# Optimization experiments

Measured on AMD Instinct MI355X. Metric: run time of the kernel, lower is better.

Reference implementation:

```python
import jax, jax.numpy as jnp
import numpy as np

NUM_EMBEDDINGS = 1024
EMBEDDING_DIM = 256


def setup_inputs() -> dict:
    key = jax.random.key(0)
    k1, k2 = jax.random.split(key)
    z = jax.random.normal(k1, (32, EMBEDDING_DIM, 32, 32), dtype=jnp.float32)
    codebook = jax.random.normal(k2, (NUM_EMBEDDINGS, EMBEDDING_DIM), dtype=jnp.float32)
    return {"z": z, "codebook": codebook}


def reference(z, codebook):
    # z: (B, C, H, W) -> (B, H, W, C) -> (B*H*W, C)
    B, C, H, W = z.shape
    z_bhwc = jnp.transpose(z, (0, 2, 3, 1))
    z_flat = z_bhwc.reshape(-1, C)  # (N, C)

    # pairwise squared distances: ||z||^2 + ||e||^2 - 2 z.e^T  -> (N, K)
    distances = (
        jnp.sum(z_flat ** 2, axis=1, keepdims=True)
        + jnp.sum(codebook ** 2, axis=1)
        - 2.0 * jnp.matmul(z_flat, codebook.T)
    )
    argmin_codewords = jnp.argmin(distances, axis=1)  # (N,)
    min_codewords = jax.nn.one_hot(argmin_codewords, NUM_EMBEDDINGS, dtype=jnp.float32)  # (N, K)

    # quantized latents via one-hot @ codebook, back to (B, C, H, W)
    z_quantized = jnp.matmul(min_codewords, codebook).reshape(B, H, W, C)
    z_quantized = jnp.transpose(z_quantized, (0, 3, 1, 2))
    return (min_codewords, z_quantized)
```

## Files before the change

kernel.cpp:

```cpp
#include <hip/hip_runtime.h>

#define N_ROWS 32768
#define K_CODES 1024
#define CDIM 256

typedef _Float16 half8 __attribute__((ext_vector_type(8)));
typedef _Float16 half4 __attribute__((ext_vector_type(4)));
typedef float floatx16 __attribute__((ext_vector_type(16)));
typedef unsigned long long ull;

#define WS_ZH   0ull
#define WS_ZL   16777216ull
#define WS_CBH  33554432ull
#define WS_CBL  34078720ull
#define WS_CBN  34603008ull
#define WS_PART 34607104ull
#define WS_IDX  36704256ull
#define WS_NEED 36835328ull

__device__ __forceinline__ void g2lds16(const void* g, void* l) {
    __builtin_amdgcn_global_load_lds(
        (const __attribute__((address_space(1))) void*)g,
        (__attribute__((address_space(3))) void*)l, 16, 0, 0);
}

__global__ __launch_bounds__(256) void prep_all(const float* __restrict__ z,
                                                const float* __restrict__ cb,
                                                _Float16* __restrict__ zh,
                                                _Float16* __restrict__ zl,
                                                _Float16* __restrict__ cbh,
                                                _Float16* __restrict__ cbl,
                                                float* __restrict__ cbn) {
    __shared__ float t[64][68];
    if (blockIdx.x >= 2048) {
        int k = ((blockIdx.x - 2048) << 2) | (threadIdx.x >> 6);
        int lane = threadIdx.x & 63;
        float4 v = reinterpret_cast<const float4*>(cb + k * CDIM)[lane];
        float s0 = v.x * 32.f, s1 = v.y * 32.f, s2 = v.z * 32.f, s3 = v.w * 32.f;
        half4 hv, lv;
        hv[0] = (_Float16)s0; lv[0] = (_Float16)(s0 - (float)hv[0]);
        hv[1] = (_Float16)s1; lv[1] = (_Float16)(s1 - (float)hv[1]);
        hv[2] = (_Float16)s2; lv[2] = (_Float16)(s2 - (float)hv[2]);
        hv[3] = (_Float16)s3; lv[3] = (_Float16)(s3 - (float)hv[3]);
        size_t off = (size_t)((lane >> 1) * K_CODES + k) * 8 + ((lane & 1) * 4);
        *reinterpret_cast<half4*>(&cbh[off]) = hv;
        *reinterpret_cast<half4*>(&cbl[off]) = lv;
        float s = s0 * s0 + s1 * s1 + s2 * s2 + s3 * s3;
        #pragma unroll
        for (int off2 = 32; off2 > 0; off2 >>= 1) s += __shfl_down(s, off2);
        if (lane == 0) cbn[k] = s;
        return;
    }
    int hwt = blockIdx.x & 15;
    int ct  = (blockIdx.x >> 4) & 3;
    int bb  = blockIdx.x >> 6;
    int tid = threadIdx.x;
    #pragma unroll
    for (int p = 0; p < 4; p++) {
        int e = p * 256 + tid;
        int c = e >> 4, h4 = e & 15;
        float4 v = *reinterpret_cast<const float4*>(
            &z[((bb * 256 + ct * 64 + c) << 10) + hwt * 64 + h4 * 4]);
        *reinterpret_cast<float4*>(&t[c][h4 * 4]) = v;
    }
    __syncthreads();
    #pragma unroll
    for (int p = 0; p < 4; p++) {
        int e = p * 256 + tid;
        int hw = e >> 4, c4 = e & 15;
        half4 hv, lv;
        #pragma unroll
        for (int j = 0; j < 4; j++) {
            float s = t[c4 * 4 + j][hw] * 32.f;
            _Float16 h = (_Float16)s;
            hv[j] = h;
            lv[j] = (_Float16)(s - (float)h);
        }
        int n = bb * 1024 + hwt * 64 + hw;
        int cg = ct * 64 + c4 * 4;
        size_t off = (size_t)((cg >> 3) * N_ROWS + n) * 8 + (cg & 7);
        *reinterpret_cast<half4*>(&zh[off]) = hv;
        *reinterpret_cast<half4*>(&zl[off]) = lv;
    }
}

__global__ __launch_bounds__(256, 4) void vq_mfma32(
    const _Float16* __restrict__ zh, const _Float16* __restrict__ zl,
    const _Float16* __restrict__ cbh, const _Float16* __restrict__ cbl,
    const float* __restrict__ cbn, ull* __restrict__ partial) {

    __shared__ _Float16 AhL[4096], AlL[4096], BhL[4096], BlL[4096];
    __shared__ float rvv[128][2];
    __shared__ int   rcc[128][2];

    const int tid = threadIdx.x;
    const int lane = tid & 63, wave = tid >> 6;
    const int wm = wave & 1, wn = wave >> 1;
    const int fm = lane & 31, fq = lane >> 5;
    const int L = (blockIdx.x & 7) * 256 + (blockIdx.x >> 3);
    const int codeTile = L & 7;
    const int rowTile  = L >> 3;
    const int rowBase = rowTile * 128, codeBase = codeTile * 128;

    floatx16 acc[4];
    #pragma unroll
    for (int i = 0; i < 4; i++) acc[i] = (floatx16)0.f;

    for (int cc = 0; cc < 8; cc++) {
        #pragma unroll
        for (int i = 0; i < 2; i++) {
            int G = i * 256 + tid;
            int q = G >> 7, r = G & 127;
            size_t ao = ((size_t)(cc * 4 + q) * N_ROWS + rowBase + r) * 8;
            size_t bo = ((size_t)(cc * 4 + q) * K_CODES + codeBase + r) * 8;
            g2lds16(zh + ao,  &AhL[G * 8]);
            g2lds16(zl + ao,  &AlL[G * 8]);
            g2lds16(cbh + bo, &BhL[G * 8]);
            g2lds16(cbl + bo, &BlL[G * 8]);
        }
        __syncthreads();
        #pragma unroll
        for (int s = 0; s < 2; s++) {
            int q = s * 2 + fq;
            half8 ah[2], al[2], bh[2], bl[2];
            #pragma unroll
            for (int i = 0; i < 2; i++) {
                int ga = q * 128 + wm * 64 + i * 32 + fm;
                ah[i] = *reinterpret_cast<const half8*>(&AhL[ga * 8]);
                al[i] = *reinterpret_cast<const half8*>(&AlL[ga * 8]);
            }
            #pragma unroll
            for (int j = 0; j < 2; j++) {
                int gb = q * 128 + wn * 64 + j * 32 + fm;
                bh[j] = *reinterpret_cast<const half8*>(&BhL[gb * 8]);
                bl[j] = *reinterpret_cast<const half8*>(&BlL[gb * 8]);
            }
            #pragma unroll
            for (int i = 0; i < 2; i++)
                #pragma unroll
                for (int j = 0; j < 2; j++) {
                    acc[i*2+j] = __builtin_amdgcn_mfma_f32_32x32x16_f16(ah[i], bh[j], acc[i*2+j], 0, 0, 0);
                    acc[i*2+j] = __builtin_amdgcn_mfma_f32_32x32x16_f16(al[i], bh[j], acc[i*2+j], 0, 0, 0);
                    acc[i*2+j] = __builtin_amdgcn_mfma_f32_32x32x16_f16(ah[i], bl[j], acc[i*2+j], 0, 0, 0);
                }
        }
        __syncthreads();
    }

    float cbnv[2];
    #pragma unroll
    for (int j = 0; j < 2; j++) cbnv[j] = cbn[codeBase + wn * 64 + j * 32 + fm];

    #pragma unroll
    for (int i = 0; i < 2; i++)
        #pragma unroll
        for (int r = 0; r < 16; r++) {
            float best = 3.4e38f; int bcode = 0x7fffffff;
            #pragma unroll
            for (int j = 0; j < 2; j++) {
                float d = fmaf(-2.f, acc[i*2+j][r], cbnv[j]);
                int code = codeBase + wn * 64 + j * 32 + fm;
                if (d < best) { best = d; bcode = code; }
            }
            #pragma unroll
            for (int m = 1; m < 32; m <<= 1) {
                float ov = __shfl_xor(best, m, 64);
                int   oc = __shfl_xor(bcode, m, 64);
                if (ov < best || (ov == best && oc < bcode)) { best = ov; bcode = oc; }
            }
            if (fm == 0) {
                int row = wm * 64 + i * 32 + (r & 3) + 8 * (r >> 2) + 4 * fq;
                rvv[row][wn] = best;
                rcc[row][wn] = bcode;
            }
        }
    __syncthreads();
    if (tid < 128) {
        float v0 = rvv[tid][0]; int c0 = rcc[tid][0];
        float v1 = rvv[tid][1]; int c1 = rcc[tid][1];
        if (v1 < v0 || (v1 == v0 && c1 < c0)) { v0 = v1; c0 = c1; }
        unsigned u = __float_as_uint(v0);
        u = (u & 0x80000000u) ? ~u : (u | 0x80000000u);
        partial[(size_t)(rowBase + tid) * 8 + codeTile] =
            ((ull)u << 32) | (unsigned)c0;
    }
}

__global__ __launch_bounds__(256) void onehot_fin2(const ull* __restrict__ partial,
                                                   int* __restrict__ idx,
                                                   float* __restrict__ out) {
    __shared__ int sid[16];
    const int rb = blockIdx.x * 16;
    const int tid = threadIdx.x;
    if (tid < 128) {
        ull v = partial[(size_t)rb * 8 + tid];
        #pragma unroll
        for (int m = 1; m < 8; m <<= 1) {
            ull o = __shfl_xor(v, m, 64);
            if (o < v) v = o;
        }
        if ((tid & 7) == 0) {
            int r = tid >> 3;
            int id = (int)(v & 0xffffffffu);
            sid[r] = id;
            idx[rb + r] = id;
        }
    }
    __syncthreads();
    const int k4 = tid << 2;
    #pragma unroll
    for (int r = 0; r < 16; r++) {
        int id = sid[r];
        float4 v4;
        v4.x = (k4     == id) ? 1.f : 0.f;
        v4.y = (k4 + 1 == id) ? 1.f : 0.f;
        v4.z = (k4 + 2 == id) ? 1.f : 0.f;
        v4.w = (k4 + 3 == id) ? 1.f : 0.f;
        reinterpret_cast<float4*>(out)[(size_t)(rb + r) * 256 + tid] = v4;
    }
}

__global__ __launch_bounds__(256) void zq_fill2(const int* __restrict__ idx,
                                                const float* __restrict__ cb,
                                                float* __restrict__ out) {
    __shared__ float tile[64][257];
    const int tid = threadIdx.x;
    const int n0 = (blockIdx.x >> 2) << 8;
    const int c0 = (blockIdx.x & 3) << 6;
    const int b  = n0 >> 10;
    const int hw0 = n0 & 1023;

    const int id = idx[n0 + tid];
    const float4* cb4 = reinterpret_cast<const float4*>(cb);
    #pragma unroll
    for (int jj = 0; jj < 16; jj++) {
        float4 v = cb4[id * 64 + (c0 >> 2) + jj];
        tile[jj * 4 + 0][tid] = v.x;
        tile[jj * 4 + 1][tid] = v.y;
        tile[jj * 4 + 2][tid] = v.z;
        tile[jj * 4 + 3][tid] = v.w;
    }
    __syncthreads();
    #pragma unroll
    for (int c = 0; c < 64; c++) {
        out[((size_t)(b * 256 + c0 + c) << 10) + hw0 + tid] = tile[c][tid];
    }
}


__global__ __launch_bounds__(64) void cb_norms(const float* __restrict__ cb,
                                               float* __restrict__ cbn) {
    int k = blockIdx.x;
    int lane = threadIdx.x;
    float4 v = reinterpret_cast<const float4*>(cb + k * CDIM)[lane];
    float s = v.x * v.x + v.y * v.y + v.z * v.z + v.w * v.w;
    #pragma unroll
    for (int off = 32; off > 0; off >>= 1) s += __shfl_down(s, off);
    if (lane == 0) cbn[k] = s;
}

__global__ __launch_bounds__(256) void cb_transpose(const float* __restrict__ cb,
                                                    float* __restrict__ cbt) {
    __shared__ float t[32][33];
    int k0 = (blockIdx.x & 31) * 32;
    int c0 = (blockIdx.x >> 5) * 32;
    int lane = threadIdx.x & 31;
    int row = threadIdx.x >> 5;
    #pragma unroll
    for (int s = 0; s < 4; s++) {
        int r = row + s * 8;
        t[r][lane] = cb[(k0 + r) * CDIM + c0 + lane];
    }
    __syncthreads();
    #pragma unroll
    for (int s = 0; s < 4; s++) {
        int r = row + s * 8;
        cbt[(c0 + r) * K_CODES + k0 + lane] = t[lane][r];
    }
}

__global__ __launch_bounds__(512, 2) void vq_argmin(const float* __restrict__ z,
                                                    const float* __restrict__ cbt,
                                                    const float* __restrict__ cbn,
                                                    int* __restrict__ idx_out) {
    __shared__ float As[64][128];
    __shared__ float Bs[64][256];

    const int tid = threadIdx.x;
    const int tx = tid & 31;
    const int ty = tid >> 5;
    const int rowBase = blockIdx.x * 128;
    const int bb = rowBase >> 10;
    const int hwBase = rowBase & 1023;

    float minv[8];
    int   mini[8];
    #pragma unroll
    for (int i = 0; i < 8; i++) { minv[i] = 3.4e38f; mini[i] = 0; }

    for (int kt = 0; kt < K_CODES; kt += 256) {
        float acc[2][2][4][4];
        #pragma unroll
        for (int a = 0; a < 2; a++)
            #pragma unroll
            for (int b = 0; b < 2; b++)
                #pragma unroll
                for (int i = 0; i < 4; i++)
                    #pragma unroll
                    for (int j = 0; j < 4; j++) acc[a][b][i][j] = 0.f;

        for (int ccb = 0; ccb < CDIM; ccb += 64) {
            #pragma unroll
            for (int l = 0; l < 4; l++) {
                int f = tid + l * 512;
                int r4 = f & 31, c = f >> 5;
                float4 v = *reinterpret_cast<const float4*>(
                    &z[((bb * 256 + ccb + c) << 10) + hwBase + r4 * 4]);
                *reinterpret_cast<float4*>(&As[c][r4 * 4]) = v;
            }
            #pragma unroll
            for (int l = 0; l < 8; l++) {
                int f = tid + l * 512;
                int k4 = f & 63, c = f >> 6;
                float4 v = *reinterpret_cast<const float4*>(
                    &cbt[(ccb + c) * K_CODES + kt + k4 * 4]);
                *reinterpret_cast<float4*>(&Bs[c][k4 * 4]) = v;
            }
            __syncthreads();
            #pragma unroll 4
            for (int c = 0; c < 64; c++) {
                float4 a0 = *reinterpret_cast<const float4*>(&As[c][ty * 4]);
                float4 a1 = *reinterpret_cast<const float4*>(&As[c][64 + ty * 4]);
                float4 b0 = *reinterpret_cast<const float4*>(&Bs[c][tx * 4]);
                float4 b1 = *reinterpret_cast<const float4*>(&Bs[c][128 + tx * 4]);
                float av[2][4] = {{a0.x, a0.y, a0.z, a0.w}, {a1.x, a1.y, a1.z, a1.w}};
                float bw[2][4] = {{b0.x, b0.y, b0.z, b0.w}, {b1.x, b1.y, b1.z, b1.w}};
                #pragma unroll
                for (int ri = 0; ri < 2; ri++)
                    #pragma unroll
                    for (int i = 0; i < 4; i++)
                        #pragma unroll
                        for (int ci = 0; ci < 2; ci++)
                            #pragma unroll
                            for (int j = 0; j < 4; j++)
                                acc[ri][ci][i][j] =
                                    fmaf(av[ri][i], bw[ci][j], acc[ri][ci][i][j]);
            }
            __syncthreads();
        }
        #pragma unroll
        for (int ci = 0; ci < 2; ci++)
            #pragma unroll
            for (int j = 0; j < 4; j++) {
                int code = kt + ci * 128 + tx * 4 + j;
                float nrm = cbn[code];
                #pragma unroll
                for (int ri = 0; ri < 2; ri++)
                    #pragma unroll
                    for (int i = 0; i < 4; i++) {
                        float d = fmaf(-2.f, acc[ri][ci][i][j], nrm);
                        int r = ri * 4 + i;
                        if (d < minv[r]) { minv[r] = d; mini[r] = code; }
                    }
            }
    }

    __syncthreads();
    float (*rv)[32] = reinterpret_cast<float(*)[32]>(&As[0][0]);
    int   (*rix)[32] = reinterpret_cast<int(*)[32]>(&As[32][0]);
    #pragma unroll
    for (int ri = 0; ri < 2; ri++)
        #pragma unroll
        for (int i = 0; i < 4; i++) {
            int row = ri * 64 + ty * 4 + i;
            rv[row][tx] = minv[ri * 4 + i];
            rix[row][tx] = mini[ri * 4 + i];
        }
    __syncthreads();
    if (tid < 128) {
        float bvv = rv[tid][0]; int bii = rix[tid][0];
        #pragma unroll
        for (int t = 1; t < 32; t++) {
            float v = rv[tid][t]; int ii = rix[tid][t];
            if (v < bvv || (v == bvv && ii < bii)) { bvv = v; bii = ii; }
        }
        idx_out[rowBase + tid] = bii;
    }
}

__global__ __launch_bounds__(256) void onehot_fill(const int* __restrict__ idx,
                                                   float* __restrict__ out) {
    int i = blockIdx.x * 256 + threadIdx.x;
    int n  = i >> 8;
    int k4 = (i & 255) << 2;
    int id = idx[n];
    float4 v;
    v.x = (k4     == id) ? 1.f : 0.f;
    v.y = (k4 + 1 == id) ? 1.f : 0.f;
    v.z = (k4 + 2 == id) ? 1.f : 0.f;
    v.w = (k4 + 3 == id) ? 1.f : 0.f;
    reinterpret_cast<float4*>(out)[i] = v;
}

extern "C" void kernel_launch(void* const* d_in, const int* in_sizes, int n_in,
                              void* d_out, int out_size, void* d_ws, size_t ws_size,
                              hipStream_t stream) {
    const float* z  = (const float*)d_in[0];
    const float* cb = (const float*)d_in[1];
    float* out0 = (float*)d_out;
    float* out1 = out0 + (size_t)N_ROWS * K_CODES;

    if (ws_size >= WS_NEED) {
        _Float16* zh  = (_Float16*)((char*)d_ws + WS_ZH);
        _Float16* zl  = (_Float16*)((char*)d_ws + WS_ZL);
        _Float16* cbh = (_Float16*)((char*)d_ws + WS_CBH);
        _Float16* cbl = (_Float16*)((char*)d_ws + WS_CBL);
        float* cbn = (float*)((char*)d_ws + WS_CBN);
        ull* part = (ull*)((char*)d_ws + WS_PART);
        int* idx = (int*)((char*)d_ws + WS_IDX);

        prep_all<<<2304, 256, 0, stream>>>(z, cb, zh, zl, cbh, cbl, cbn);
        vq_mfma32<<<2048, 256, 0, stream>>>(zh, zl, cbh, cbl, cbn, part);
        onehot_fin2<<<2048, 256, 0, stream>>>(part, idx, out0);
        zq_fill2<<<512, 256, 0, stream>>>(idx, cb, out1);
    } else {
        float* cbn = (float*)d_ws;
        int*   idx = (int*)((char*)d_ws + 4096);
        float* cbt = (float*)((char*)d_ws + 4096 + 131072);

        cb_norms<<<K_CODES, 64, 0, stream>>>(cb, cbn);
        cb_transpose<<<256, 256, 0, stream>>>(cb, cbt);
        vq_argmin<<<N_ROWS / 128, 512, 0, stream>>>(z, cbt, cbn, idx);
        onehot_fill<<<(N_ROWS * K_CODES / 4) / 256, 256, 0, stream>>>(idx, out0);
        zq_fill2<<<512, 256, 0, stream>>>(idx, cb, out1);
    }
}
```

Measured before the change: 279.5 us.

## Keep codebook slice resident in LDS, stream z from global, reduce argmin with atomicMin

```diff
diff --git a/kernel.cpp b/kernel.cpp
--- a/kernel.cpp
+++ b/kernel.cpp
@@ -30,7 +30,8 @@
                                                 _Float16* __restrict__ zl,
                                                 _Float16* __restrict__ cbh,
                                                 _Float16* __restrict__ cbl,
-                                                float* __restrict__ cbn) {
+                                                float* __restrict__ cbn,
+                                                ull* __restrict__ part) {
     __shared__ float t[64][68];
     if (blockIdx.x >= 2048) {
         int k = ((blockIdx.x - 2048) << 2) | (threadIdx.x >> 6);
@@ -51,6 +52,8 @@
         if (lane == 0) cbn[k] = s;
         return;
     }
+    if (threadIdx.x < 16) part[blockIdx.x * 16 + threadIdx.x] = ~0ull;
+
     int hwt = blockIdx.x & 15;
     int ct  = (blockIdx.x >> 4) & 3;
     int bb  = blockIdx.x >> 6;
@@ -84,56 +87,58 @@
     }
 }
 
-__global__ __launch_bounds__(256, 4) void vq_mfma32(
+__global__ __launch_bounds__(256, 2) void vq_breg(
     const _Float16* __restrict__ zh, const _Float16* __restrict__ zl,
     const _Float16* __restrict__ cbh, const _Float16* __restrict__ cbl,
-    const float* __restrict__ cbn, ull* __restrict__ partial) {
-
-    __shared__ _Float16 AhL[4096], AlL[4096], BhL[4096], BlL[4096];
-    __shared__ float rvv[128][2];
-    __shared__ int   rcc[128][2];
+    const float* __restrict__ cbn, ull* __restrict__ part) {
+
+    __shared__ _Float16 BhL[16384], BlL[16384];
 
     const int tid = threadIdx.x;
-    const int lane = tid & 63, wave = tid >> 6;
-    const int wm = wave & 1, wn = wave >> 1;
+    const int lane = tid & 63, w = tid >> 6;
     const int fm = lane & 31, fq = lane >> 5;
     const int L = (blockIdx.x & 7) * 256 + (blockIdx.x >> 3);
-    const int codeTile = L & 7;
-    const int rowTile  = L >> 3;
-    const int rowBase = rowTile * 128, codeBase = codeTile * 128;
+    const int codeTile = L & 15;
+    const int rowTile  = L >> 4;
+    const int rowBase = rowTile * 256, codeBase = codeTile * 64;
+
+    #pragma unroll
+    for (int p = 0; p < 8; p++) {
+        int G = p * 256 + tid;
+        int plane = G >> 6, code = G & 63;
+        size_t so = ((size_t)plane * K_CODES + codeBase + code) * 8;
+        g2lds16(cbh + so, &BhL[G * 8]);
+        g2lds16(cbl + so, &BlL[G * 8]);
+    }
+
+    float cbnv[2];
+    #pragma unroll
+    for (int j = 0; j < 2; j++) cbnv[j] = cbn[codeBase + j * 32 + fm];
 
     floatx16 acc[4];
     #pragma unroll
     for (int i = 0; i < 4; i++) acc[i] = (floatx16)0.f;
 
+    __syncthreads();
+
+    const int rw = rowBase + w * 64;
+    #pragma unroll
     for (int cc = 0; cc < 8; cc++) {
         #pragma unroll
-        for (int i = 0; i < 2; i++) {
-            int G = i * 256 + tid;
-            int q = G >> 7, r = G & 127;
-            size_t ao = ((size_t)(cc * 4 + q) * N_ROWS + rowBase + r) * 8;
-            size_t bo = ((size_t)(cc * 4 + q) * K_CODES + codeBase + r) * 8;
-            g2lds16(zh + ao,  &AhL[G * 8]);
-            g2lds16(zl + ao,  &AlL[G * 8]);
-            g2lds16(cbh + bo, &BhL[G * 8]);
-            g2lds16(cbl + bo, &BlL[G * 8]);
-        }
-        __syncthreads();
-        #pragma unroll
         for (int s = 0; s < 2; s++) {
-            int q = s * 2 + fq;
+            const int plane = cc * 4 + s * 2 + fq;
             half8 ah[2], al[2], bh[2], bl[2];
             #pragma unroll
             for (int i = 0; i < 2; i++) {
-                int ga = q * 128 + wm * 64 + i * 32 + fm;
-                ah[i] = *reinterpret_cast<const half8*>(&AhL[ga * 8]);
-                al[i] = *reinterpret_cast<const half8*>(&AlL[ga * 8]);
+                size_t ao = ((size_t)plane * N_ROWS + rw + i * 32 + fm) * 8;
+                ah[i] = *reinterpret_cast<const half8*>(&zh[ao]);
+                al[i] = *reinterpret_cast<const half8*>(&zl[ao]);
             }
             #pragma unroll
             for (int j = 0; j < 2; j++) {
-                int gb = q * 128 + wn * 64 + j * 32 + fm;
-                bh[j] = *reinterpret_cast<const half8*>(&BhL[gb * 8]);
-                bl[j] = *reinterpret_cast<const half8*>(&BlL[gb * 8]);
+                int gb = (plane * 64 + j * 32 + fm) * 8;
+                bh[j] = *reinterpret_cast<const half8*>(&BhL[gb]);
+                bl[j] = *reinterpret_cast<const half8*>(&BlL[gb]);
             }
             #pragma unroll
             for (int i = 0; i < 2; i++)
@@ -144,12 +149,7 @@
                     acc[i*2+j] = __builtin_amdgcn_mfma_f32_32x32x16_f16(ah[i], bl[j], acc[i*2+j], 0, 0, 0);
                 }
         }
-        __syncthreads();
-    }
-
-    float cbnv[2];
-    #pragma unroll
-    for (int j = 0; j < 2; j++) cbnv[j] = cbn[codeBase + wn * 64 + j * 32 + fm];
+    }
 
     #pragma unroll
     for (int i = 0; i < 2; i++)
@@ -159,7 +159,7 @@
             #pragma unroll
             for (int j = 0; j < 2; j++) {
                 float d = fmaf(-2.f, acc[i*2+j][r], cbnv[j]);
-                int code = codeBase + wn * 64 + j * 32 + fm;
+                int code = codeBase + j * 32 + fm;
                 if (d < best) { best = d; bcode = code; }
             }
             #pragma unroll
@@ -169,42 +169,24 @@
                 if (ov < best || (ov == best && oc < bcode)) { best = ov; bcode = oc; }
             }
             if (fm == 0) {
-                int row = wm * 64 + i * 32 + (r & 3) + 8 * (r >> 2) + 4 * fq;
-                rvv[row][wn] = best;
-                rcc[row][wn] = bcode;
-            }
-        }
-    __syncthreads();
-    if (tid < 128) {
-        float v0 = rvv[tid][0]; int c0 = rcc[tid][0];
-        float v1 = rvv[tid][1]; int c1 = rcc[tid][1];
-        if (v1 < v0 || (v1 == v0 && c1 < c0)) { v0 = v1; c0 = c1; }
-        unsigned u = __float_as_uint(v0);
-        u = (u & 0x80000000u) ? ~u : (u | 0x80000000u);
-        partial[(size_t)(rowBase + tid) * 8 + codeTile] =
-            ((ull)u << 32) | (unsigned)c0;
-    }
-}
-
-__global__ __launch_bounds__(256) void onehot_fin2(const ull* __restrict__ partial,
+                int row = rw + i * 32 + (r & 3) + 8 * (r >> 2) + 4 * fq;
+                unsigned u = __float_as_uint(best);
+                u = (u & 0x80000000u) ? ~u : (u | 0x80000000u);
+                atomicMin(&part[row], ((ull)u << 32) | (unsigned)bcode);
+            }
+        }
+}
+
+__global__ __launch_bounds__(256) void onehot_fin3(const ull* __restrict__ part,
                                                    int* __restrict__ idx,
                                                    float* __restrict__ out) {
     __shared__ int sid[16];
     const int rb = blockIdx.x * 16;
     const int tid = threadIdx.x;
-    if (tid < 128) {
-        ull v = partial[(size_t)rb * 8 + tid];
-        #pragma unroll
-        for (int m = 1; m < 8; m <<= 1) {
-            ull o = __shfl_xor(v, m, 64);
-            if (o < v) v = o;
-        }
-        if ((tid & 7) == 0) {
-            int r = tid >> 3;
-            int id = (int)(v & 0xffffffffu);
-            sid[r] = id;
-            idx[rb + r] = id;
-        }
+    if (tid < 16) {
+        int id = (int)(part[rb + tid] & 0xffffffffu);
+        sid[tid] = id;
+        idx[rb + tid] = id;
     }
     __syncthreads();
     const int k4 = tid << 2;
@@ -419,9 +401,9 @@
         ull* part = (ull*)((char*)d_ws + WS_PART);
         int* idx = (int*)((char*)d_ws + WS_IDX);
 
-        prep_all<<<2304, 256, 0, stream>>>(z, cb, zh, zl, cbh, cbl, cbn);
-        vq_mfma32<<<2048, 256, 0, stream>>>(zh, zl, cbh, cbl, cbn, part);
-        onehot_fin2<<<2048, 256, 0, stream>>>(part, idx, out0);
+        prep_all<<<2304, 256, 0, stream>>>(z, cb, zh, zl, cbh, cbl, cbn, part);
+        vq_breg<<<2048, 256, 0, stream>>>(zh, zl, cbh, cbl, cbn, part);
+        onehot_fin3<<<2048, 256, 0, stream>>>(part, idx, out0);
         zq_fill2<<<512, 256, 0, stream>>>(idx, cb, out1);
     } else {
         float* cbn = (float*)d_ws;
```

Measured after the change: 320.5 us. +14.7%, slower.
